# Kernel optimization log

Hardware: AMD Instinct MI355X
Metric: run time of the kernel (lower is better)

## Reference

```python
import jax, jax.numpy as jnp
import numpy as np

B, N, H, NH = 2, 2048, 1024, 16
HD = H // NH


def setup_inputs() -> dict:
    key = jax.random.key(0)
    ks = jax.random.split(key, 12)
    s = 0.02
    inp = {
        "q": jax.random.normal(ks[0], (B, N, H), jnp.float32),
        "k": jax.random.normal(ks[1], (B, N, H), jnp.float32),
        "v": jax.random.normal(ks[2], (B, N, H), jnp.float32),
        # causal mask, broadcast over batch and heads
        "mask": jnp.tril(jnp.ones((N, N), jnp.float32))[None, None, :, :],
        "Wq": jax.random.normal(ks[3], (H, H), jnp.float32) * s,
        "bq": jnp.zeros((H,), jnp.float32),
        "Wk": jax.random.normal(ks[4], (H, H), jnp.float32) * s,
        "bk": jnp.zeros((H,), jnp.float32),
        "Wv": jax.random.normal(ks[5], (H, H), jnp.float32) * s,
        "bv": jnp.zeros((H,), jnp.float32),
        "Wp": jax.random.normal(ks[6], (H, H), jnp.float32) * s,
        "bp": jnp.zeros((H,), jnp.float32),
    }
    return inp


def _split_heads(x):
    # [b, n, (h d)] -> [b, h, n, d]
    b, n, _ = x.shape
    return x.reshape(b, n, NH, HD).transpose(0, 2, 1, 3)


def reference(q, k, v, mask, Wq, bq, Wk, bk, Wv, bv, Wp, bp):
    Q = _split_heads(q @ Wq.T + bq)                      # [b,h,n,d]
    K = _split_heads(k @ Wk.T + bk)
    V = _split_heads(v @ Wv.T + bv)
    scores = jnp.einsum("bhnd,bhmd->bhnm", Q, K) / jnp.sqrt(jnp.float32(HD))
    scores = jnp.where(mask == 0, -jnp.inf, scores)
    attn = jax.nn.softmax(scores, axis=-1)
    out = jnp.einsum("bhnm,bhmd->bhnd", attn, V)         # [b,h,n,d]
    out = out.transpose(0, 2, 1, 3).reshape(q.shape[0], q.shape[1], H)
    # dropout is identity in eval mode
    return out @ Wp.T + bp
```

## Files before the change

kernel.cpp:

```cpp
#include <hip/hip_runtime.h>


typedef unsigned short ushortT;
typedef unsigned int uintT;
typedef __attribute__((ext_vector_type(8))) short short8;
typedef __attribute__((ext_vector_type(4))) float f32x4;

#define M_ROWS 4096
#define KDIM   1024
#define NDIM   1024
#define SEQ    2048
#define HDHEAD 64

__device__ __forceinline__ float bf2f(ushortT s) {
    union { unsigned u; float f; } v; v.u = ((unsigned)s) << 16; return v.f;
}
__device__ __forceinline__ ushortT f2bf(float x) {
    union { float f; unsigned u; } v; v.f = x;
    return (ushortT)((v.u + 0x7fffu + ((v.u >> 16) & 1u)) >> 16);
}

__device__ __forceinline__ bool detect_f32(const uintT* w) {
    int hits = 0;
#pragma unroll
    for (int i = 0; i < 16; ++i) {
        const unsigned e = (w[i] >> 7) & 0xffu;
        hits += (e >= 118u && e <= 131u) ? 1 : 0;
    }
    return hits < 8;
}

__device__ __forceinline__ short8 cvt8(const float* p) {
    f32x4 a = *(const f32x4*)p;
    f32x4 b = *(const f32x4*)(p + 4);
    short8 r;
    r[0] = (short)f2bf(a[0]); r[1] = (short)f2bf(a[1]);
    r[2] = (short)f2bf(a[2]); r[3] = (short)f2bf(a[3]);
    r[4] = (short)f2bf(b[0]); r[5] = (short)f2bf(b[1]);
    r[6] = (short)f2bf(b[2]); r[7] = (short)f2bf(b[3]);
    return r;
}

__device__ __forceinline__ void gl2lds16(const ushortT* g, ushortT* l) {
    __builtin_amdgcn_global_load_lds(
        (const __attribute__((address_space(1))) void*)g,
        (__attribute__((address_space(3))) void*)l,
        16, 0, 0);
}

__device__ __forceinline__ void bar_lgkm() {
    __builtin_amdgcn_sched_barrier(0);
    asm volatile("s_waitcnt lgkmcnt(0)" ::: "memory");
    __builtin_amdgcn_s_barrier();
    __builtin_amdgcn_sched_barrier(0);
}

__global__ __launch_bounds__(256) void convert_kernel(
    const void* __restrict__ q, const void* __restrict__ k, const void* __restrict__ v,
    const void* __restrict__ Wq, const void* __restrict__ Wk,
    const void* __restrict__ Wv, const void* __restrict__ Wp,
    const void* __restrict__ bq, const void* __restrict__ bk,
    const void* __restrict__ bv, const void* __restrict__ bp,
    ushortT* __restrict__ dst) {
    const bool f32m = detect_f32((const uintT*)q);
    const size_t u = (size_t)blockIdx.x * 256 + threadIdx.x;

    const void* src; size_t soff, doff;
    if (u < 1572864u) {
        const int seg = (int)(u >> 19);
        const size_t o = u & 524287u;
        src  = seg == 0 ? q : (seg == 1 ? k : v);
        soff = o * 8;
        doff = (size_t)seg * 4194304u + o * 8;
    } else if (u < 2097152u) {
        const size_t u2 = u - 1572864u;
        const int seg = (int)(u2 >> 17);
        const size_t o = u2 & 131071u;
        src  = seg == 0 ? Wq : (seg == 1 ? Wk : (seg == 2 ? Wv : Wp));
        soff = o * 8;
        doff = 12582912u + (size_t)seg * 1048576u + o * 8;
    } else {
        const size_t u3 = u - 2097152u;
        const int seg = (int)(u3 >> 7);
        const size_t o = u3 & 127u;
        src  = seg == 0 ? bq : (seg == 1 ? bk : (seg == 2 ? bv : bp));
        soff = o * 8;
        doff = 16777216u + (size_t)seg * 1024u + o * 8;
    }

    if (f32m)
        *(short8*)(dst + doff) = cvt8((const float*)src + soff);
    else
        *(short8*)(dst + doff) = *(const short8*)((const ushortT*)src + soff);
}

__device__ __forceinline__ void gemm_body(const void* __restrict__ Av,
                                          const void* __restrict__ Wv_,
                                          const void* __restrict__ biasv,
                                          void* __restrict__ Cv,
                                          bool a_f32, bool w_f32, bool c_f32,
                                          float cscale, bool vt_store) {
    __shared__ ushortT ldsA[128 * 64];
    __shared__ ushortT ldsB[128 * 64];

    const int tid  = threadIdx.x;
    const int lane = tid & 63;
    const int wid  = tid >> 6;
    const int bm   = blockIdx.x;
    const int bn   = blockIdx.y;
    const int wm   = wid >> 1;
    const int wn   = wid & 1;

    const int srow = lane >> 2;
    const int scol = (lane & 3) * 8;

    f32x4 acc[4][4];
#pragma unroll
    for (int i = 0; i < 4; ++i)
#pragma unroll
        for (int j = 0; j < 4; ++j) acc[i][j] = (f32x4){0.f, 0.f, 0.f, 0.f};

    const int fr   = lane & 15;
    const int quad = lane >> 4;

    for (int kt = 0; kt < KDIM / 64; ++kt) {
        const int k0 = kt * 64;
        if (!a_f32 && !w_f32) {
#pragma unroll
            for (int t = 0; t < 4; ++t) {
                const int chunk = wid * 4 + t;
                const int kh  = chunk >> 3;
                const int r16 = (chunk & 7) * 16;
                const size_t ra = (size_t)(bm * 128 + r16 + srow) * KDIM + k0 + kh * 32 + scol;
                const size_t rw = (size_t)(bn * 128 + r16 + srow) * KDIM + k0 + kh * 32 + scol;
                gl2lds16((const ushortT*)Av + ra, ldsA + chunk * 512);
                gl2lds16((const ushortT*)Wv_ + rw, ldsB + chunk * 512);
            }
        } else {
            short8 ta[4], tb[4];
#pragma unroll
            for (int t = 0; t < 4; ++t) {
                const int chunk = wid * 4 + t;
                const int kh  = chunk >> 3;
                const int r16 = (chunk & 7) * 16;
                const size_t ra = (size_t)(bm * 128 + r16 + srow) * KDIM + k0 + kh * 32 + scol;
                const size_t rw = (size_t)(bn * 128 + r16 + srow) * KDIM + k0 + kh * 32 + scol;
                ta[t] = a_f32 ? cvt8((const float*)Av + ra)
                              : *(const short8*)((const ushortT*)Av + ra);
                tb[t] = w_f32 ? cvt8((const float*)Wv_ + rw)
                              : *(const short8*)((const ushortT*)Wv_ + rw);
            }
#pragma unroll
            for (int t = 0; t < 4; ++t) {
                const int chunk = wid * 4 + t;
                *(short8*)(ldsA + chunk * 512 + lane * 8) = ta[t];
                *(short8*)(ldsB + chunk * 512 + lane * 8) = tb[t];
            }
        }
        __syncthreads();

#pragma unroll
        for (int s = 0; s < 2; ++s) {
            short8 aF[4], bF[4];
#pragma unroll
            for (int i = 0; i < 4; ++i)
                aF[i] = *(const short8*)(ldsA + s * 4096 + (wm * 64 + i * 16 + fr) * 32 + quad * 8);
#pragma unroll
            for (int j = 0; j < 4; ++j)
                bF[j] = *(const short8*)(ldsB + s * 4096 + (wn * 64 + j * 16 + fr) * 32 + quad * 8);
#pragma unroll
            for (int i = 0; i < 4; ++i)
#pragma unroll
                for (int j = 0; j < 4; ++j)
                    acc[i][j] = __builtin_amdgcn_mfma_f32_16x16x32_bf16(aF[i], bF[j], acc[i][j], 0, 0, 0);
        }
        __syncthreads();
    }

#pragma unroll
    for (int j = 0; j < 4; ++j) {
        const int col = bn * 128 + wn * 64 + j * 16 + fr;
        const float bv = w_f32 ? ((const float*)biasv)[col]
                               : bf2f(((const ushortT*)biasv)[col]);
#pragma unroll
        for (int i = 0; i < 4; ++i) {
            const int row0 = bm * 128 + wm * 64 + i * 16 + quad * 4;
#pragma unroll
            for (int r = 0; r < 4; ++r) {
                const float val = (acc[i][j][r] + bv) * cscale;
                const int row = row0 + r;
                if (vt_store) {
                    const int bb = row >> 11, n = row & 2047;
                    const int hh = col >> 6,  d = col & 63;
                    ((ushortT*)Cv)[(size_t)((bb * 16 + hh) * 64 + d) * SEQ + n] = f2bf(val);
                } else if (c_f32) {
                    ((float*)Cv)[(size_t)row * NDIM + col] = val;
                } else {
                    ((ushortT*)Cv)[(size_t)row * NDIM + col] = f2bf(val);
                }
            }
        }
    }
}

__global__ __launch_bounds__(256, 3) void qkv_proj_kernel(
    const void* __restrict__ q, const void* __restrict__ k, const void* __restrict__ v,
    const void* __restrict__ Wq, const void* __restrict__ Wk, const void* __restrict__ Wv,
    const void* __restrict__ bq, const void* __restrict__ bk, const void* __restrict__ bv,
    ushortT* __restrict__ Qp, ushortT* __restrict__ Kp, ushortT* __restrict__ Vt) {
    const bool f32m = detect_f32((const uintT*)q);
    const void* A; const void* W; const void* bias; ushortT* C;
    float cscale = 1.f; bool vt = false;
    if (blockIdx.z == 0)      { A = q; W = Wq; bias = bq; C = Qp; cscale = 0.125f; }
    else if (blockIdx.z == 1) { A = k; W = Wk; bias = bk; C = Kp; }
    else                      { A = v; W = Wv; bias = bv; C = Vt; vt = true; }
    gemm_body(A, W, bias, (void*)C, f32m, f32m, false, cscale, vt);
}

__global__ __launch_bounds__(256, 2) void out_proj_kernel(
    const ushortT* __restrict__ A, const void* __restrict__ W,
    const void* __restrict__ bias, void* __restrict__ C,
    const void* __restrict__ qdet) {
    const bool wf = detect_f32((const uintT*)W);
    const bool cf = detect_f32((const uintT*)qdet);

    __shared__ ushortT ldsA[128 * 64];
    __shared__ ushortT ldsB[64 * 64];

    const int tid  = threadIdx.x;
    const int lane = tid & 63;
    const int wid  = tid >> 6;
    const int bm   = blockIdx.x;
    const int bn   = blockIdx.y;

    const int srow = lane >> 2;
    const int scol = (lane & 3) * 8;
    const int fr   = lane & 15;
    const int quad = lane >> 4;

    f32x4 acc[2][4];
#pragma unroll
    for (int i = 0; i < 2; ++i)
#pragma unroll
        for (int j = 0; j < 4; ++j) acc[i][j] = (f32x4){0.f, 0.f, 0.f, 0.f};

    for (int kt = 0; kt < KDIM / 64; ++kt) {
        const int k0 = kt * 64;
        if (!wf) {
#pragma unroll
            for (int t = 0; t < 4; ++t) {
                const int chunk = wid * 4 + t;
                const int kh  = chunk >> 3;
                const int r16 = (chunk & 7) * 16;
                const size_t ra = (size_t)(bm * 128 + r16 + srow) * KDIM + k0 + kh * 32 + scol;
                gl2lds16(A + ra, ldsA + chunk * 512);
            }
#pragma unroll
            for (int t = 0; t < 2; ++t) {
                const int chunk = wid * 2 + t;
                const int kh  = chunk >> 2;
                const int r16 = (chunk & 3) * 16;
                const size_t rw = (size_t)(bn * 64 + r16 + srow) * KDIM + k0 + kh * 32 + scol;
                gl2lds16((const ushortT*)W + rw, ldsB + chunk * 512);
            }
        } else {
            short8 ta[4], tb[2];
#pragma unroll
            for (int t = 0; t < 4; ++t) {
                const int chunk = wid * 4 + t;
                const int kh  = chunk >> 3;
                const int r16 = (chunk & 7) * 16;
                const size_t ra = (size_t)(bm * 128 + r16 + srow) * KDIM + k0 + kh * 32 + scol;
                ta[t] = *(const short8*)(A + ra);
            }
#pragma unroll
            for (int t = 0; t < 2; ++t) {
                const int chunk = wid * 2 + t;
                const int kh  = chunk >> 2;
                const int r16 = (chunk & 3) * 16;
                const size_t rw = (size_t)(bn * 64 + r16 + srow) * KDIM + k0 + kh * 32 + scol;
                tb[t] = cvt8((const float*)W + rw);
            }
#pragma unroll
            for (int t = 0; t < 4; ++t)
                *(short8*)(ldsA + (wid * 4 + t) * 512 + lane * 8) = ta[t];
#pragma unroll
            for (int t = 0; t < 2; ++t)
                *(short8*)(ldsB + (wid * 2 + t) * 512 + lane * 8) = tb[t];
        }
        __syncthreads();

#pragma unroll
        for (int s = 0; s < 2; ++s) {
            short8 aF[2], bF[4];
#pragma unroll
            for (int i = 0; i < 2; ++i)
                aF[i] = *(const short8*)(ldsA + s * 4096 + (wid * 32 + i * 16 + fr) * 32 + quad * 8);
#pragma unroll
            for (int j = 0; j < 4; ++j)
                bF[j] = *(const short8*)(ldsB + s * 2048 + (j * 16 + fr) * 32 + quad * 8);
#pragma unroll
            for (int i = 0; i < 2; ++i)
#pragma unroll
                for (int j = 0; j < 4; ++j)
                    acc[i][j] = __builtin_amdgcn_mfma_f32_16x16x32_bf16(aF[i], bF[j], acc[i][j], 0, 0, 0);
        }
        __syncthreads();
    }

#pragma unroll
    for (int j = 0; j < 4; ++j) {
        const int col = bn * 64 + j * 16 + fr;
        const float bv = wf ? ((const float*)bias)[col]
                            : bf2f(((const ushortT*)bias)[col]);
#pragma unroll
        for (int i = 0; i < 2; ++i) {
            const int row0 = bm * 128 + wid * 32 + i * 16 + quad * 4;
#pragma unroll
            for (int r = 0; r < 4; ++r) {
                const float val = acc[i][j][r] + bv;
                const int row = row0 + r;
                if (cf) ((float*)C)[(size_t)row * NDIM + col] = val;
                else    ((ushortT*)C)[(size_t)row * NDIM + col] = f2bf(val);
            }
        }
    }
}

__global__ __launch_bounds__(256, 4) void flash_attn_kernel(
    const ushortT* __restrict__ Qp, const ushortT* __restrict__ Kp,
    const ushortT* __restrict__ Vt, ushortT* __restrict__ Op) {
    __shared__ ushortT ldsK[2 * 64 * 40];
    __shared__ ushortT ldsV[64 * 72];
    __shared__ ushortT ldsP[4][16 * 72];

    const int tid  = threadIdx.x;
    const int lane = tid & 63;
    const int wid  = tid >> 6;
    const int fr   = lane & 15;
    const int quad = lane >> 4;

    const int lin = blockIdx.x;
    const int c   = lin & 255;
    const int g   = lin >> 8;
    const int bh  = c & 31;
    const int t   = c >> 5;
    int qb;
    if      (g == 0) qb = t;
    else if (g == 1) qb = 31 - t;
    else if (g == 2) qb = 15 - t;
    else             qb = 16 + t;
    const int h = bh & 15;
    const int b = bh >> 4;

    const size_t base = (size_t)b * SEQ * NDIM + (size_t)h * HDHEAD;
    const size_t vtb  = (size_t)(b * 16 + h) * HDHEAD * SEQ;

    int ksst[2], keyloc[2];
#pragma unroll
    for (int u = 0; u < 2; ++u) {
        const int chunk = wid * 2 + u;
        ksst[u]   = chunk >> 2;
        keyloc[u] = (chunk & 3) * 16 + (lane >> 2);
    }
    const int c8 = (lane & 3) * 8;
    const int vd  = lane >> 3;
    const int vk8 = (lane & 7) * 8;

    const int q0  = qb * 64;
    const int nkv = qb + 1;

    short8 qf[2];
#pragma unroll
    for (int ks = 0; ks < 2; ++ks)
        qf[ks] = *(const short8*)(Qp + base + (size_t)(q0 + wid * 16 + fr) * NDIM + ks * 32 + quad * 8);

    f32x4 accO[4];
#pragma unroll
    for (int dt = 0; dt < 4; ++dt) accO[dt] = (f32x4){0.f, 0.f, 0.f, 0.f};
    float lsum[4];
#pragma unroll
    for (int r = 0; r < 4; ++r) lsum[r] = 0.f;

    short8 kreg[2], vreg[2];
#pragma unroll
    for (int u = 0; u < 2; ++u) {
        kreg[u] = *(const short8*)(Kp + base + (size_t)keyloc[u] * NDIM + ksst[u] * 32 + c8);
        const int d = (wid * 2 + u) * 8 + vd;
        vreg[u] = *(const short8*)(Vt + vtb + (size_t)d * SEQ + vk8);
    }

    const int qi = q0 + wid * 16 + quad * 4;

    for (int kt = 0; kt < nkv; ++kt) {
        bar_lgkm();

#pragma unroll
        for (int u = 0; u < 2; ++u) {
            *(short8*)(ldsK + ksst[u] * 2560 + keyloc[u] * 40 + c8) = kreg[u];
            const int d = (wid * 2 + u) * 8 + vd;
            *(short8*)(ldsV + d * 72 + vk8) = vreg[u];
        }

        if (kt + 1 < nkv) {
            const int kv1 = (kt + 1) * 64;
#pragma unroll
            for (int u = 0; u < 2; ++u) {
                kreg[u] = *(const short8*)(Kp + base + (size_t)(kv1 + keyloc[u]) * NDIM + ksst[u] * 32 + c8);
                const int d = (wid * 2 + u) * 8 + vd;
                vreg[u] = *(const short8*)(Vt + vtb + (size_t)d * SEQ + kv1 + vk8);
            }
        }
        bar_lgkm();

        f32x4 s[4];
#pragma unroll
        for (int nt = 0; nt < 4; ++nt) {
            f32x4 a = (f32x4){0.f, 0.f, 0.f, 0.f};
#pragma unroll
            for (int ks = 0; ks < 2; ++ks) {
                short8 kf = *(const short8*)(ldsK + ks * 2560 + (nt * 16 + fr) * 40 + quad * 8);
                a = __builtin_amdgcn_mfma_f32_16x16x32_bf16(qf[ks], kf, a, 0, 0, 0);
            }
            s[nt] = a;
        }

        const int kv0 = kt * 64;
        if (kt == nkv - 1) {
#pragma unroll
            for (int nt = 0; nt < 4; ++nt) {
                const int kj = kv0 + nt * 16 + fr;
#pragma unroll
                for (int r = 0; r < 4; ++r)
                    s[nt][r] = (kj > qi + r) ? -1e30f : s[nt][r];
            }
        }

        ushortT* pbuf = ldsP[wid];
#pragma unroll
        for (int nt = 0; nt < 4; ++nt) {
#pragma unroll
            for (int r = 0; r < 4; ++r) {
                const float p = __expf(fminf(s[nt][r], 30.f));
                lsum[r] += p;
                pbuf[(quad * 4 + r) * 72 + nt * 16 + fr] = f2bf(p);
            }
        }

        asm volatile("" ::: "memory");

#pragma unroll
        for (int ks = 0; ks < 2; ++ks) {
            short8 pf = *(const short8*)(pbuf + fr * 72 + ks * 32 + quad * 8);
#pragma unroll
            for (int dt = 0; dt < 4; ++dt) {
                short8 vf = *(const short8*)(ldsV + (dt * 16 + fr) * 72 + ks * 32 + quad * 8);
                accO[dt] = __builtin_amdgcn_mfma_f32_16x16x32_bf16(pf, vf, accO[dt], 0, 0, 0);
            }
        }
    }

#pragma unroll
    for (int r = 0; r < 4; ++r) {
#pragma unroll
        for (int off = 8; off >= 1; off >>= 1)
            lsum[r] += __shfl_xor(lsum[r], off, 64);
    }
#pragma unroll
    for (int dt = 0; dt < 4; ++dt) {
#pragma unroll
        for (int r = 0; r < 4; ++r) {
            const size_t row = (size_t)(q0 + wid * 16 + quad * 4 + r);
            Op[(size_t)b * SEQ * NDIM + row * NDIM + h * HDHEAD + dt * 16 + fr] =
                f2bf(accO[dt][r] / lsum[r]);
        }
    }
}

extern "C" void kernel_launch(void* const* d_in, const int* in_sizes, int n_in,
                              void* d_out, int out_size, void* d_ws, size_t ws_size,
                              hipStream_t stream) {
    const void* q  = d_in[0];
    const void* k  = d_in[1];
    const void* v  = d_in[2];
    const void* Wq = d_in[4];
    const void* bq = d_in[5];
    const void* Wk = d_in[6];
    const void* bk = d_in[7];
    const void* Wv = d_in[8];
    const void* bv = d_in[9];
    const void* Wp = d_in[10];
    const void* bp = d_in[11];

    dim3 blk(256);
    const size_t FAST_WS = 58728448;

    if (ws_size >= FAST_WS) {
        ushortT* cb   = (ushortT*)d_ws;
        ushortT* qb16 = cb;
        ushortT* kb16 = cb + 4194304u;
        ushortT* vb16 = cb + 8388608u;
        ushortT* Wqb  = cb + 12582912u;
        ushortT* Wkb  = cb + 13631488u;
        ushortT* Wvb  = cb + 14680064u;
        ushortT* Wpb  = cb + 15728640u;
        ushortT* bqb  = cb + 16777216u;
        ushortT* bkb  = cb + 16778240u;
        ushortT* bvb  = cb + 16779264u;
        ushortT* bpb  = cb + 16780288u;
        ushortT* Qp   = cb + 16781312u;
        ushortT* Kp   = Qp + 4194304u;
        ushortT* Vt   = Kp + 4194304u;
        ushortT* Op   = qb16;

        convert_kernel<<<dim3(8194), blk, 0, stream>>>(
            q, k, v, Wq, Wk, Wv, Wp, bq, bk, bv, bp, cb);
        qkv_proj_kernel<<<dim3(32, 8, 3), blk, 0, stream>>>(
            qb16, kb16, vb16, Wqb, Wkb, Wvb, bqb, bkb, bvb, Qp, Kp, Vt);
        flash_attn_kernel<<<dim3(1024), blk, 0, stream>>>(Qp, Kp, Vt, Op);
        out_proj_kernel<<<dim3(32, 16), blk, 0, stream>>>(Op, Wpb, bpb, d_out, q);
    } else {
        ushortT* ws = (ushortT*)d_ws;
        ushortT* Qp = ws;
        ushortT* Kp = ws + (size_t)M_ROWS * NDIM;
        ushortT* Vt = ws + (size_t)2 * M_ROWS * NDIM;
        ushortT* Op = ws + (size_t)3 * M_ROWS * NDIM;

        qkv_proj_kernel<<<dim3(32, 8, 3), blk, 0, stream>>>(
            q, k, v, Wq, Wk, Wv, bq, bk, bv, Qp, Kp, Vt);
        flash_attn_kernel<<<dim3(1024), blk, 0, stream>>>(Qp, Kp, Vt, Op);
        out_proj_kernel<<<dim3(32, 16), blk, 0, stream>>>(Op, Wp, bp, d_out, q);
    }
}
```

Before: 233.4 us.

## Double-buffer K/V tiles in LDS to drop one barrier per iteration

Doubles the shared-memory buffers for K and V tiles. The next tile is written into the alternate buffer after the current tile's MFMAs, which removes one of the two block barriers per key-value iteration. Shared memory grows, so occupancy per CU drops and the launch bounds go from 4 to 3 blocks. Register lifetime of the prefetched tiles also gets longer.

```diff
diff --git a/kernel.cpp b/kernel.cpp
--- a/kernel.cpp
+++ b/kernel.cpp
@@ -327,11 +327,11 @@
     }
 }
 
-__global__ __launch_bounds__(256, 4) void flash_attn_kernel(
+__global__ __launch_bounds__(256, 3) void flash_attn_kernel(
     const ushortT* __restrict__ Qp, const ushortT* __restrict__ Kp,
     const ushortT* __restrict__ Vt, ushortT* __restrict__ Op) {
-    __shared__ ushortT ldsK[2 * 64 * 40];
-    __shared__ ushortT ldsV[64 * 72];
+    __shared__ ushortT ldsK[2][2 * 64 * 40];
+    __shared__ ushortT ldsV[2][64 * 72];
     __shared__ ushortT ldsP[4][16 * 72];
 
     const int tid  = threadIdx.x;
@@ -389,20 +389,20 @@
         const int d = (wid * 2 + u) * 8 + vd;
         vreg[u] = *(const short8*)(Vt + vtb + (size_t)d * SEQ + vk8);
     }
+#pragma unroll
+    for (int u = 0; u < 2; ++u) {
+        *(short8*)(ldsK[0] + ksst[u] * 2560 + keyloc[u] * 40 + c8) = kreg[u];
+        const int d = (wid * 2 + u) * 8 + vd;
+        *(short8*)(ldsV[0] + d * 72 + vk8) = vreg[u];
+    }
 
     const int qi = q0 + wid * 16 + quad * 4;
 
     for (int kt = 0; kt < nkv; ++kt) {
-        bar_lgkm();
-
-#pragma unroll
-        for (int u = 0; u < 2; ++u) {
-            *(short8*)(ldsK + ksst[u] * 2560 + keyloc[u] * 40 + c8) = kreg[u];
-            const int d = (wid * 2 + u) * 8 + vd;
-            *(short8*)(ldsV + d * 72 + vk8) = vreg[u];
-        }
-
-        if (kt + 1 < nkv) {
+        const int p = kt & 1;
+        const bool more = (kt + 1 < nkv);
+
+        if (more) {
             const int kv1 = (kt + 1) * 64;
 #pragma unroll
             for (int u = 0; u < 2; ++u) {
@@ -411,7 +411,11 @@
                 vreg[u] = *(const short8*)(Vt + vtb + (size_t)d * SEQ + kv1 + vk8);
             }
         }
+
         bar_lgkm();
+
+        const ushortT* bK = ldsK[p];
+        const ushortT* bV = ldsV[p];
 
         f32x4 s[4];
 #pragma unroll
@@ -419,7 +423,7 @@
             f32x4 a = (f32x4){0.f, 0.f, 0.f, 0.f};
 #pragma unroll
             for (int ks = 0; ks < 2; ++ks) {
-                short8 kf = *(const short8*)(ldsK + ks * 2560 + (nt * 16 + fr) * 40 + quad * 8);
+                short8 kf = *(const short8*)(bK + ks * 2560 + (nt * 16 + fr) * 40 + quad * 8);
                 a = __builtin_amdgcn_mfma_f32_16x16x32_bf16(qf[ks], kf, a, 0, 0, 0);
             }
             s[nt] = a;
@@ -441,9 +445,9 @@
         for (int nt = 0; nt < 4; ++nt) {
 #pragma unroll
             for (int r = 0; r < 4; ++r) {
-                const float p = __expf(fminf(s[nt][r], 30.f));
-                lsum[r] += p;
-                pbuf[(quad * 4 + r) * 72 + nt * 16 + fr] = f2bf(p);
+                const float pe = __expf(fminf(s[nt][r], 30.f));
+                lsum[r] += pe;
+                pbuf[(quad * 4 + r) * 72 + nt * 16 + fr] = f2bf(pe);
             }
         }
 
@@ -454,8 +458,19 @@
             short8 pf = *(const short8*)(pbuf + fr * 72 + ks * 32 + quad * 8);
 #pragma unroll
             for (int dt = 0; dt < 4; ++dt) {
-                short8 vf = *(const short8*)(ldsV + (dt * 16 + fr) * 72 + ks * 32 + quad * 8);
+                short8 vf = *(const short8*)(bV + (dt * 16 + fr) * 72 + ks * 32 + quad * 8);
                 accO[dt] = __builtin_amdgcn_mfma_f32_16x16x32_bf16(pf, vf, accO[dt], 0, 0, 0);
+            }
+        }
+
+        if (more) {
+            ushortT* oK = ldsK[p ^ 1];
+            ushortT* oV = ldsV[p ^ 1];
+#pragma unroll
+            for (int u = 0; u < 2; ++u) {
+                *(short8*)(oK + ksst[u] * 2560 + keyloc[u] * 40 + c8) = kreg[u];
+                const int d = (wid * 2 + u) * 8 + vd;
+                *(short8*)(oV + d * 72 + vk8) = vreg[u];
             }
         }
     }
```

Result: no change. 237.2 us (+1.6%).
